# Performance work log

Measured on AMD Instinct MI355X. Metric: run time of the kernel, lower is better.

## Reference

```python
import jax, jax.numpy as jnp
import numpy as np
from jax import lax

_MS_SSIM_WEIGHTS = [0.0448, 0.2856, 0.3001, 0.2363, 0.1333]
LEVELS = 5
WINDOW_SIZE = 11
SIGMA = 1.5
DATA_RANGE = 2.0


def _gaussian_kernel(size, sigma, channels):
    x = jnp.arange(size, dtype=jnp.float32) - size // 2
    g = jnp.exp(-x ** 2 / (2.0 * sigma ** 2))
    g = g / g.sum()
    k2d = jnp.outer(g, g)  # [size, size]
    # depthwise kernel: [C, 1, size, size] (OIHW with feature_group_count=C)
    return jnp.broadcast_to(k2d[None, None], (channels, 1, size, size))


def _depthwise_conv(x, kernel, pad):
    C = x.shape[1]
    return lax.conv_general_dilated(
        x, kernel,
        window_strides=(1, 1),
        padding=[(pad, pad), (pad, pad)],
        dimension_numbers=('NCHW', 'OIHW', 'NCHW'),
        feature_group_count=C)


def _avg_pool2(x):
    s = lax.reduce_window(x, 0.0, lax.add, (1, 1, 2, 2), (1, 1, 2, 2), 'VALID')
    return s * 0.25


def _ssim(x, y, window_size=WINDOW_SIZE, sigma=SIGMA, data_range=DATA_RANGE):
    K1, K2 = 0.01, 0.03
    C1 = (K1 * data_range) ** 2
    C2 = (K2 * data_range) ** 2
    kernel = _gaussian_kernel(window_size, sigma, x.shape[1])
    pad = window_size // 2
    mu1 = _depthwise_conv(x, kernel, pad)
    mu2 = _depthwise_conv(y, kernel, pad)
    mu1_sq = mu1 * mu1
    mu2_sq = mu2 * mu2
    mu1_mu2 = mu1 * mu2
    sig1_sq = _depthwise_conv(x * x, kernel, pad) - mu1_sq
    sig2_sq = _depthwise_conv(y * y, kernel, pad) - mu2_sq
    sig12 = _depthwise_conv(x * y, kernel, pad) - mu1_mu2
    num = (2.0 * mu1_mu2 + C1) * (2.0 * sig12 + C2)
    den = (mu1_sq + mu2_sq + C1) * (sig1_sq + sig2_sq + C2)
    ssim_map = num / (den + 1e-8)
    return ssim_map.mean()


def setup_inputs() -> dict:
    key = jax.random.key(0)
    k1, k2 = jax.random.split(key)
    pred = jax.random.normal(k1, (16, 3, 512, 512), dtype=jnp.float32)
    target = jax.random.normal(k2, (16, 3, 512, 512), dtype=jnp.float32)
    return {"pred": pred, "target": target}


def reference(pred, target):
    weights = jnp.asarray(_MS_SSIM_WEIGHTS[:LEVELS], dtype=jnp.float32)
    weights = weights / weights.sum()
    ms_ssim_val = jnp.zeros((), dtype=jnp.float32)
    x, y = pred, target
    for i in range(LEVELS):
        s = _ssim(x, y)
        ms_ssim_val = ms_ssim_val + weights[i] * s
        if i < LEVELS - 1:
            x = _avg_pool2(x)
            y = _avg_pool2(y)
    return 1.0 - ms_ssim_val
```

## Files before the change

### kernel.cpp

```cpp
#include <hip/hip_runtime.h>


#define TW 64
#define NIMG 48
#define HPITCH 62
#define NSLOT 256
#define SSTRIDE 16

template <int TH>
__global__ __launch_bounds__(256, 3) void ssim_level_kernel(
    const float* __restrict__ x, const float* __restrict__ y,
    long imgStride, int rowStride,
    float* __restrict__ dsx, float* __restrict__ dsy,
    long dsImgStride, int dsRowStride,
    const float* __restrict__ zpad,
    float* __restrict__ slots, int H, int W, int pad, int do_ds)
{
    constexpr int HHALO = TH + 10;
    constexpr int PLANE = HHALO * HPITCH;

    const float G[11] = {
        0.00102839f, 0.00759877f, 0.03600077f, 0.10936069f, 0.21300539f,
        0.26601173f, 0.21300539f, 0.10936069f, 0.03600077f, 0.00759877f,
        0.00102839f};
    const float C1 = 4.0e-4f;
    const float C2 = 3.6e-3f;

    __shared__ __align__(16) float hfT[5 * PLANE];

    const int t   = threadIdx.x;
    const int img = blockIdx.z;
    const int C0  = blockIdx.x * TW;
    const int R0  = blockIdx.y * TH;
    const float* xi = x + (long)img * imgStride;
    const float* yi = y + (long)img * imgStride;

    if (do_ds) {
        const int dsW = W >> 1, dsH = H >> 1;
        const int dr = t >> 5, dc = t & 31;
        const int gr2 = (R0 >> 1) + dr;
        const int gc2 = (C0 >> 1) + dc;
        const long dbase = (long)img * dsImgStride;
        if (dr < (TH >> 1) && gr2 < dsH && gc2 < dsW) {
            const float* sx = xi + (long)(2 * gr2) * rowStride + 2 * gc2;
            const float* sy = yi + (long)(2 * gr2) * rowStride + 2 * gc2;
            const float2 a0 = *reinterpret_cast<const float2*>(sx);
            const float2 a1 = *reinterpret_cast<const float2*>(sx + rowStride);
            const float2 b0 = *reinterpret_cast<const float2*>(sy);
            const float2 b1 = *reinterpret_cast<const float2*>(sy + rowStride);
            const long o = dbase + (long)gr2 * dsRowStride + gc2;
            dsx[o] = 0.25f * (a0.x + a0.y + a1.x + a1.y);
            dsy[o] = 0.25f * (b0.x + b0.y + b1.x + b1.y);
        }
        if (dr < (TH >> 1) && gr2 < dsH && dc < 8) {
            if (blockIdx.x == 0) {
                const long o = dbase + (long)gr2 * dsRowStride + (dc - 8);
                dsx[o] = 0.0f; dsy[o] = 0.0f;
            }
            if (blockIdx.x == gridDim.x - 1) {
                const long o = dbase + (long)gr2 * dsRowStride + (dsW + dc);
                dsx[o] = 0.0f; dsy[o] = 0.0f;
            }
        }
    }

    if (t < HHALO * (TW / 8)) {
        const int r  = t % HHALO;
        const int q  = t / HHALO;
        const int gr = R0 + r - 5;
        const bool rok = ((unsigned)gr < (unsigned)H);
        const int gc0 = C0 + (q << 3) - 8;
        const bool fastp = pad || ((C0 >= 8) && (C0 + TW + 8 <= W));

        float xv[24], yv[24];
        if (fastp) {
            const float* px = rok ? (xi + (long)gr * rowStride + gc0) : zpad;
            const float* py = rok ? (yi + (long)gr * rowStride + gc0) : zpad;
#pragma unroll
            for (int v = 0; v < 6; ++v) {
                const float4 a = reinterpret_cast<const float4*>(px)[v];
                const float4 b = reinterpret_cast<const float4*>(py)[v];
                xv[4 * v + 0] = a.x; xv[4 * v + 1] = a.y;
                xv[4 * v + 2] = a.z; xv[4 * v + 3] = a.w;
                yv[4 * v + 0] = b.x; yv[4 * v + 1] = b.y;
                yv[4 * v + 2] = b.z; yv[4 * v + 3] = b.w;
            }
        } else {
            const float* xrow = xi + (long)gr * rowStride;
            const float* yrow = yi + (long)gr * rowStride;
#pragma unroll
            for (int k = 3; k < 21; ++k) {
                const int gc = gc0 + k;
                const bool ok = rok && ((unsigned)gc < (unsigned)W);
                xv[k] = ok ? xrow[gc] : 0.0f;
                yv[k] = ok ? yrow[gc] : 0.0f;
            }
        }

        float xx[18], yy[18], xy[18];
#pragma unroll
        for (int k = 0; k < 18; ++k) {
            const float a = xv[k + 3], b = yv[k + 3];
            xx[k] = a * a; yy[k] = b * b; xy[k] = a * b;
        }

        float hx[8], hy[8], hxx[8], hyy[8], hxy[8];
#pragma unroll
        for (int j = 0; j < 8; ++j) {
            float sx = 0.f, sy = 0.f, sxx = 0.f, syy = 0.f, sxy = 0.f;
#pragma unroll
            for (int k = 0; k < 11; ++k) {
                const float g = G[k];
                sx  = fmaf(g, xv[j + k + 3], sx);
                sy  = fmaf(g, yv[j + k + 3], sy);
                sxx = fmaf(g, xx[j + k], sxx);
                syy = fmaf(g, yy[j + k], syy);
                sxy = fmaf(g, xy[j + k], sxy);
            }
            hx[j] = sx; hy[j] = sy; hxx[j] = sxx; hyy[j] = syy; hxy[j] = sxy;
        }
        float* hp = &hfT[r * HPITCH + (q << 3)];
#pragma unroll
        for (int p = 0; p < 4; ++p) {
            reinterpret_cast<float2*>(hp + 0 * PLANE)[p] = make_float2(hx[2*p],  hx[2*p+1]);
            reinterpret_cast<float2*>(hp + 1 * PLANE)[p] = make_float2(hy[2*p],  hy[2*p+1]);
            reinterpret_cast<float2*>(hp + 2 * PLANE)[p] = make_float2(hxx[2*p], hxx[2*p+1]);
            reinterpret_cast<float2*>(hp + 3 * PLANE)[p] = make_float2(hyy[2*p], hyy[2*p+1]);
            reinterpret_cast<float2*>(hp + 4 * PLANE)[p] = make_float2(hxy[2*p], hxy[2*p+1]);
        }
    }
    __syncthreads();

    const int c   = t & 63;
    const int rr0 = (t >> 6) * (TH / 4);
    float acc[5][TH / 4];
#pragma unroll
    for (int f = 0; f < 5; ++f) {
        const float* hp = &hfT[f * PLANE + rr0 * HPITCH + c];
        float hv[10 + TH / 4];
#pragma unroll
        for (int k = 0; k < 10 + TH / 4; ++k) hv[k] = hp[k * HPITCH];
#pragma unroll
        for (int i = 0; i < TH / 4; ++i) {
            float a = 0.f;
#pragma unroll
            for (int k = 0; k < 11; ++k) a = fmaf(G[k], hv[i + k], a);
            acc[f][i] = a;
        }
    }

    float local = 0.f;
    const int gc = C0 + c;
#pragma unroll
    for (int i = 0; i < TH / 4; ++i) {
        const int gr2 = R0 + rr0 + i;
        if (gr2 < H && gc < W) {
            const float mu1 = acc[0][i], mu2 = acc[1][i];
            const float mu1s = mu1 * mu1, mu2s = mu2 * mu2, m12 = mu1 * mu2;
            const float s1  = acc[2][i] - mu1s;
            const float s2  = acc[3][i] - mu2s;
            const float s12 = acc[4][i] - m12;
            const float num = (2.f * m12 + C1) * (2.f * s12 + C2);
            const float den = (mu1s + mu2s + C1) * (s1 + s2 + C2);
            local += num * __builtin_amdgcn_rcpf(den + 1e-8f);
        }
    }

#pragma unroll
    for (int off = 32; off > 0; off >>= 1) local += __shfl_down(local, off, 64);
    if ((t & 63) == 0) {
        const int bid = (blockIdx.z * gridDim.y + blockIdx.y) * gridDim.x + blockIdx.x;
        const int slot = ((bid << 2) | (t >> 6)) & (NSLOT - 1);
        atomicAdd(slots + slot * SSTRIDE, local);
    }
}

__global__ void finalize_kernel(const float* __restrict__ slots,
                                float* __restrict__ out)
{
    const int t = threadIdx.x;
    const float w[5] = {0.0448f, 0.2856f, 0.3001f, 0.2363f, 0.1333f};
    const float wsum = w[0] + w[1] + w[2] + w[3] + w[4];
    float acc = 0.f;
#pragma unroll
    for (int lvl = 0; lvl < 5; ++lvl) {
        const int d = 512 >> lvl;
        const float cnt = (float)NIMG * (float)d * (float)d;
        acc += (w[lvl] / wsum) / cnt * slots[(lvl * NSLOT + t) * SSTRIDE];
    }
#pragma unroll
    for (int off = 32; off > 0; off >>= 1) acc += __shfl_down(acc, off, 64);
    __shared__ float p[4];
    if ((t & 63) == 0) p[t >> 6] = acc;
    __syncthreads();
    if (t == 0) out[0] = 1.0f - (p[0] + p[1] + p[2] + p[3]);
}

extern "C" void kernel_launch(void* const* d_in, const int* in_sizes, int n_in,
                              void* d_out, int out_size, void* d_ws, size_t ws_size,
                              hipStream_t stream)
{
    const float* pred = (const float*)d_in[0];
    const float* targ = (const float*)d_in[1];
    float* out = (float*)d_out;
    float* ws  = (float*)d_ws;

    const long S1 = 256L * 272, S2 = 128L * 144, S3 = 64L * 80, S4 = 32L * 48;

    float* slots = ws;
    float* zpad  = slots + 5 * NSLOT * SSTRIDE;
    float* x1 = zpad + 640;
    float* y1 = x1 + NIMG * S1;
    float* x2 = y1 + NIMG * S1;
    float* y2 = x2 + NIMG * S2;
    float* x3 = y2 + NIMG * S2;
    float* y3 = x3 + NIMG * S3;
    float* x4 = y3 + NIMG * S3;
    float* y4 = x4 + NIMG * S4;

    hipMemsetAsync(ws, 0, (size_t)(5 * NSLOT * SSTRIDE + 640) * sizeof(float), stream);

    { dim3 g(8, 32, NIMG);
      ssim_level_kernel<16><<<g, 256, 0, stream>>>(pred, targ, 512L * 512, 512,
          x1 + 8, y1 + 8, S1, 272, zpad, slots + 0 * NSLOT * SSTRIDE, 512, 512, 0, 1); }
    { dim3 g(4, 16, NIMG);
      ssim_level_kernel<16><<<g, 256, 0, stream>>>(x1 + 8, y1 + 8, S1, 272,
          x2 + 8, y2 + 8, S2, 144, zpad, slots + 1 * NSLOT * SSTRIDE, 256, 256, 1, 1); }
    { dim3 g(2, 16, NIMG);
      ssim_level_kernel<8><<<g, 256, 0, stream>>>(x2 + 8, y2 + 8, S2, 144,
          x3 + 8, y3 + 8, S3, 80, zpad, slots + 2 * NSLOT * SSTRIDE, 128, 128, 1, 1); }
    { dim3 g(1, 8, NIMG);
      ssim_level_kernel<8><<<g, 256, 0, stream>>>(x3 + 8, y3 + 8, S3, 80,
          x4 + 8, y4 + 8, S4, 48, zpad, slots + 3 * NSLOT * SSTRIDE, 64, 64, 1, 1); }
    { dim3 g(1, 4, NIMG);
      ssim_level_kernel<8><<<g, 256, 0, stream>>>(x4 + 8, y4 + 8, S4, 48,
          nullptr, nullptr, 0, 0, zpad, slots + 4 * NSLOT * SSTRIDE, 32, 32, 1, 0); }

    finalize_kernel<<<1, 256, 0, stream>>>(slots, out);
}
```

Measured before the change: 287.4 us.

## Use packed float2 FMA, interleaved LDS planes, and taller tiles for top levels

Reorganizes the shared-memory intermediate into interleaved (mu_x,mu_y) and (xx,yy) float2 planes plus a scalar xy plane, and rewrites both separable passes with 2-wide vector math so the compiler can emit packed FMA. Tile height for the first two pyramid levels doubles to 32, which cuts halo overhead, and the loader/downsample loops become strided so 256 threads can cover the larger tile. Launch bounds drop to 2 blocks per SM, accepting lower occupancy in exchange for more registers and LDS per block.

```diff
diff --git a/kernel.cpp b/kernel.cpp
--- a/kernel.cpp
+++ b/kernel.cpp
@@ -3,12 +3,15 @@
 
 #define TW 64
 #define NIMG 48
-#define HPITCH 62
+#define P2 63
+#define P1 62
 #define NSLOT 256
 #define SSTRIDE 16
 
+typedef float v2f __attribute__((ext_vector_type(2)));
+
 template <int TH>
-__global__ __launch_bounds__(256, 3) void ssim_level_kernel(
+__global__ __launch_bounds__(256, 2) void ssim_level_kernel(
     const float* __restrict__ x, const float* __restrict__ y,
     long imgStride, int rowStride,
     float* __restrict__ dsx, float* __restrict__ dsy,
@@ -17,7 +20,7 @@
     float* __restrict__ slots, int H, int W, int pad, int do_ds)
 {
     constexpr int HHALO = TH + 10;
-    constexpr int PLANE = HHALO * HPITCH;
+    constexpr int RPT   = TH / 4;
 
     const float G[11] = {
         0.00102839f, 0.00759877f, 0.03600077f, 0.10936069f, 0.21300539f,
@@ -26,7 +29,9 @@
     const float C1 = 4.0e-4f;
     const float C2 = 3.6e-3f;
 
-    __shared__ __align__(16) float hfT[5 * PLANE];
+    __shared__ __align__(16) v2f   sm01[HHALO * P2];
+    __shared__ __align__(16) v2f   sm23[HHALO * P2];
+    __shared__ __align__(16) float sm4 [HHALO * P1];
 
     const int t   = threadIdx.x;
     const int img = blockIdx.z;
@@ -37,40 +42,42 @@
 
     if (do_ds) {
         const int dsW = W >> 1, dsH = H >> 1;
-        const int dr = t >> 5, dc = t & 31;
-        const int gr2 = (R0 >> 1) + dr;
-        const int gc2 = (C0 >> 1) + dc;
         const long dbase = (long)img * dsImgStride;
-        if (dr < (TH >> 1) && gr2 < dsH && gc2 < dsW) {
-            const float* sx = xi + (long)(2 * gr2) * rowStride + 2 * gc2;
-            const float* sy = yi + (long)(2 * gr2) * rowStride + 2 * gc2;
-            const float2 a0 = *reinterpret_cast<const float2*>(sx);
-            const float2 a1 = *reinterpret_cast<const float2*>(sx + rowStride);
-            const float2 b0 = *reinterpret_cast<const float2*>(sy);
-            const float2 b1 = *reinterpret_cast<const float2*>(sy + rowStride);
-            const long o = dbase + (long)gr2 * dsRowStride + gc2;
-            dsx[o] = 0.25f * (a0.x + a0.y + a1.x + a1.y);
-            dsy[o] = 0.25f * (b0.x + b0.y + b1.x + b1.y);
-        }
-        if (dr < (TH >> 1) && gr2 < dsH && dc < 8) {
-            if (blockIdx.x == 0) {
-                const long o = dbase + (long)gr2 * dsRowStride + (dc - 8);
-                dsx[o] = 0.0f; dsy[o] = 0.0f;
-            }
-            if (blockIdx.x == gridDim.x - 1) {
-                const long o = dbase + (long)gr2 * dsRowStride + (dsW + dc);
-                dsx[o] = 0.0f; dsy[o] = 0.0f;
-            }
-        }
-    }
-
-    if (t < HHALO * (TW / 8)) {
-        const int r  = t % HHALO;
-        const int q  = t / HHALO;
+        for (int i = t; i < (TH / 2) * 32; i += 256) {
+            const int dr = i >> 5, dc = i & 31;
+            const int gr2 = (R0 >> 1) + dr;
+            const int gc2 = (C0 >> 1) + dc;
+            if (gr2 < dsH && gc2 < dsW) {
+                const float* sx = xi + (long)(2 * gr2) * rowStride + 2 * gc2;
+                const float* sy = yi + (long)(2 * gr2) * rowStride + 2 * gc2;
+                const float2 a0 = *reinterpret_cast<const float2*>(sx);
+                const float2 a1 = *reinterpret_cast<const float2*>(sx + rowStride);
+                const float2 b0 = *reinterpret_cast<const float2*>(sy);
+                const float2 b1 = *reinterpret_cast<const float2*>(sy + rowStride);
+                const long o = dbase + (long)gr2 * dsRowStride + gc2;
+                dsx[o] = 0.25f * (a0.x + a0.y + a1.x + a1.y);
+                dsy[o] = 0.25f * (b0.x + b0.y + b1.x + b1.y);
+            }
+            if (gr2 < dsH && dc < 8) {
+                if (blockIdx.x == 0) {
+                    const long o = dbase + (long)gr2 * dsRowStride + (dc - 8);
+                    dsx[o] = 0.0f; dsy[o] = 0.0f;
+                }
+                if (blockIdx.x == gridDim.x - 1) {
+                    const long o = dbase + (long)gr2 * dsRowStride + (dsW + dc);
+                    dsx[o] = 0.0f; dsy[o] = 0.0f;
+                }
+            }
+        }
+    }
+
+    const bool fastp = pad || ((C0 >= 8) && (C0 + TW + 8 <= W));
+    for (int s = t; s < HHALO * 8; s += 256) {
+        const int r  = s % HHALO;
+        const int q  = s / HHALO;
         const int gr = R0 + r - 5;
         const bool rok = ((unsigned)gr < (unsigned)H);
         const int gc0 = C0 + (q << 3) - 8;
-        const bool fastp = pad || ((C0 >= 8) && (C0 + TW + 8 <= W));
 
         float xv[24], yv[24];
         if (fastp) {
@@ -97,69 +104,83 @@
             }
         }
 
-        float xx[18], yy[18], xy[18];
+        v2f w2[18]; float xy[18];
 #pragma unroll
         for (int k = 0; k < 18; ++k) {
             const float a = xv[k + 3], b = yv[k + 3];
-            xx[k] = a * a; yy[k] = b * b; xy[k] = a * b;
-        }
-
-        float hx[8], hy[8], hxx[8], hyy[8], hxy[8];
+            v2f w; w.x = a * a; w.y = b * b;
+            w2[k] = w; xy[k] = a * b;
+        }
+
+        const int cb = (q << 3);
 #pragma unroll
         for (int j = 0; j < 8; ++j) {
-            float sx = 0.f, sy = 0.f, sxx = 0.f, syy = 0.f, sxy = 0.f;
+            v2f s01 = {0.f, 0.f}, s23 = {0.f, 0.f};
+            float s4 = 0.f;
 #pragma unroll
             for (int k = 0; k < 11; ++k) {
                 const float g = G[k];
-                sx  = fmaf(g, xv[j + k + 3], sx);
-                sy  = fmaf(g, yv[j + k + 3], sy);
-                sxx = fmaf(g, xx[j + k], sxx);
-                syy = fmaf(g, yy[j + k], syy);
-                sxy = fmaf(g, xy[j + k], sxy);
-            }
-            hx[j] = sx; hy[j] = sy; hxx[j] = sxx; hyy[j] = syy; hxy[j] = sxy;
-        }
-        float* hp = &hfT[r * HPITCH + (q << 3)];
-#pragma unroll
-        for (int p = 0; p < 4; ++p) {
-            reinterpret_cast<float2*>(hp + 0 * PLANE)[p] = make_float2(hx[2*p],  hx[2*p+1]);
-            reinterpret_cast<float2*>(hp + 1 * PLANE)[p] = make_float2(hy[2*p],  hy[2*p+1]);
-            reinterpret_cast<float2*>(hp + 2 * PLANE)[p] = make_float2(hxx[2*p], hxx[2*p+1]);
-            reinterpret_cast<float2*>(hp + 3 * PLANE)[p] = make_float2(hyy[2*p], hyy[2*p+1]);
-            reinterpret_cast<float2*>(hp + 4 * PLANE)[p] = make_float2(hxy[2*p], hxy[2*p+1]);
+                v2f w; w.x = xv[j + k + 3]; w.y = yv[j + k + 3];
+                s01 += w * g;
+                s23 += w2[j + k] * g;
+                s4   = fmaf(g, xy[j + k], s4);
+            }
+            sm01[r * P2 + cb + j] = s01;
+            sm23[r * P2 + cb + j] = s23;
+            sm4 [r * P1 + cb + j] = s4;
         }
     }
     __syncthreads();
 
     const int c   = t & 63;
-    const int rr0 = (t >> 6) * (TH / 4);
-    float acc[5][TH / 4];
-#pragma unroll
-    for (int f = 0; f < 5; ++f) {
-        const float* hp = &hfT[f * PLANE + rr0 * HPITCH + c];
-        float hv[10 + TH / 4];
-#pragma unroll
-        for (int k = 0; k < 10 + TH / 4; ++k) hv[k] = hp[k * HPITCH];
-#pragma unroll
-        for (int i = 0; i < TH / 4; ++i) {
+    const int rr0 = (t >> 6) * RPT;
+    v2f acc01[RPT], acc23[RPT];
+    float acc4[RPT];
+    {
+        v2f hv[RPT + 10];
+#pragma unroll
+        for (int k = 0; k < RPT + 10; ++k) hv[k] = sm01[(rr0 + k) * P2 + c];
+#pragma unroll
+        for (int i = 0; i < RPT; ++i) {
+            v2f a = {0.f, 0.f};
+#pragma unroll
+            for (int k = 0; k < 11; ++k) a += hv[i + k] * G[k];
+            acc01[i] = a;
+        }
+#pragma unroll
+        for (int k = 0; k < RPT + 10; ++k) hv[k] = sm23[(rr0 + k) * P2 + c];
+#pragma unroll
+        for (int i = 0; i < RPT; ++i) {
+            v2f a = {0.f, 0.f};
+#pragma unroll
+            for (int k = 0; k < 11; ++k) a += hv[i + k] * G[k];
+            acc23[i] = a;
+        }
+    }
+    {
+        float hs[RPT + 10];
+#pragma unroll
+        for (int k = 0; k < RPT + 10; ++k) hs[k] = sm4[(rr0 + k) * P1 + c];
+#pragma unroll
+        for (int i = 0; i < RPT; ++i) {
             float a = 0.f;
 #pragma unroll
-            for (int k = 0; k < 11; ++k) a = fmaf(G[k], hv[i + k], a);
-            acc[f][i] = a;
+            for (int k = 0; k < 11; ++k) a = fmaf(G[k], hs[i + k], a);
+            acc4[i] = a;
         }
     }
 
     float local = 0.f;
     const int gc = C0 + c;
 #pragma unroll
-    for (int i = 0; i < TH / 4; ++i) {
+    for (int i = 0; i < RPT; ++i) {
         const int gr2 = R0 + rr0 + i;
         if (gr2 < H && gc < W) {
-            const float mu1 = acc[0][i], mu2 = acc[1][i];
+            const float mu1 = acc01[i].x, mu2 = acc01[i].y;
             const float mu1s = mu1 * mu1, mu2s = mu2 * mu2, m12 = mu1 * mu2;
-            const float s1  = acc[2][i] - mu1s;
-            const float s2  = acc[3][i] - mu2s;
-            const float s12 = acc[4][i] - m12;
+            const float s1  = acc23[i].x - mu1s;
+            const float s2  = acc23[i].y - mu2s;
+            const float s12 = acc4[i] - m12;
             const float num = (2.f * m12 + C1) * (2.f * s12 + C2);
             const float den = (mu1s + mu2s + C1) * (s1 + s2 + C2);
             local += num * __builtin_amdgcn_rcpf(den + 1e-8f);
@@ -220,11 +241,11 @@
 
     hipMemsetAsync(ws, 0, (size_t)(5 * NSLOT * SSTRIDE + 640) * sizeof(float), stream);
 
-    { dim3 g(8, 32, NIMG);
-      ssim_level_kernel<16><<<g, 256, 0, stream>>>(pred, targ, 512L * 512, 512,
+    { dim3 g(8, 16, NIMG);
+      ssim_level_kernel<32><<<g, 256, 0, stream>>>(pred, targ, 512L * 512, 512,
           x1 + 8, y1 + 8, S1, 272, zpad, slots + 0 * NSLOT * SSTRIDE, 512, 512, 0, 1); }
-    { dim3 g(4, 16, NIMG);
-      ssim_level_kernel<16><<<g, 256, 0, stream>>>(x1 + 8, y1 + 8, S1, 272,
+    { dim3 g(4, 8, NIMG);
+      ssim_level_kernel<32><<<g, 256, 0, stream>>>(x1 + 8, y1 + 8, S1, 272,
           x2 + 8, y2 + 8, S2, 144, zpad, slots + 1 * NSLOT * SSTRIDE, 256, 256, 1, 1); }
     { dim3 g(2, 16, NIMG);
       ssim_level_kernel<8><<<g, 256, 0, stream>>>(x2 + 8, y2 + 8, S2, 144,
```

After: 283.3 us. No clear change (-1.4%).
